# Optimization experiments

Measured on AMD Instinct MI355X. Metric: run time of the kernel, lower is better.

The kernel has to match this reference:

```python
import jax, jax.numpy as jnp
import numpy as np

B, S, U = 64, 64, 16
EMB = 10
D = U - 2 + 2 * EMB      # encoder d_model = 34
DD = 3                   # decoder d_model
FF = 4                   # dim_feedforward
NL = 4                   # num layers (enc and dec)
ENH = 2                  # encoder heads
WV, SV = 10000, 400      # word / syllable vocab sizes


def _ln(x, w, b, eps=1e-5):
    mu = jnp.mean(x, -1, keepdims=True)
    var = jnp.mean((x - mu) ** 2, -1, keepdims=True)
    return (x - mu) / jnp.sqrt(var + eps) * w + b


def _mha(xq, xkv, qkv_w, qkv_b, out_w, out_b, nhead, mask=None):
    d = xq.shape[-1]
    wq, wk, wv = jnp.split(qkv_w, 3, axis=0)
    bq, bk, bv = jnp.split(qkv_b, 3, axis=0)
    q = xq @ wq.T + bq
    k = xkv @ wk.T + bk
    v = xkv @ wv.T + bv
    b_, sq, sk = q.shape[0], q.shape[1], k.shape[1]
    dh = d // nhead
    q = q.reshape(b_, sq, nhead, dh)
    k = k.reshape(b_, sk, nhead, dh)
    v = v.reshape(b_, sk, nhead, dh)
    scores = jnp.einsum('bqhd,bkhd->bhqk', q, k) * (1.0 / np.sqrt(dh))
    if mask is not None:
        scores = scores + mask
    attn = jax.nn.softmax(scores, axis=-1)
    out = jnp.einsum('bhqk,bkhd->bqhd', attn, v).reshape(b_, sq, d)
    return out @ out_w.T + out_b


def _pos_encoding(batch, d_model):
    # Faithful to the original quirk: pe has shape [max_len, 1, d] and is added
    # to a batch-first [B,S,D] tensor as x + pe[:B]  ->  row b of pe is added
    # to ALL sequence positions of batch element b.
    pos = jnp.arange(batch, dtype=jnp.float32)[:, None]
    div = jnp.exp(jnp.arange(0, d_model, 2, dtype=jnp.float32) * (-np.log(10000.0) / d_model))
    ang = pos * div  # [B, D/2]
    pe = jnp.stack([jnp.sin(ang), jnp.cos(ang)], axis=-1).reshape(batch, d_model)
    return pe[:, None, :]  # [B,1,D]


def setup_inputs() -> dict:
    key = jax.random.key(0)
    ks = iter(jax.random.split(key, 64))

    def n(shape, s=0.1):
        return jax.random.normal(next(ks), shape, dtype=jnp.float32) * s

    base = jax.random.uniform(next(ks), (B, S, U), dtype=jnp.float32)
    widx = jax.random.randint(next(ks), (B, S), 0, WV).astype(jnp.float32)
    sidx = jax.random.randint(next(ks), (B, S), 0, SV).astype(jnp.float32)
    src = base.at[:, :, U - 2].set(widx).at[:, :, U - 1].set(sidx)
    return {
        'src': src,
        'word_emb': jax.random.uniform(next(ks), (WV, EMB), jnp.float32, -0.1, 0.1),
        'syll_emb': jax.random.uniform(next(ks), (SV, EMB), jnp.float32, -0.1, 0.1),
        'enc_qkv_w': n((NL, 3 * D, D)), 'enc_qkv_b': jnp.zeros((NL, 3 * D)),
        'enc_out_w': n((NL, D, D)), 'enc_out_b': jnp.zeros((NL, D)),
        'enc_ln1_w': jnp.ones((NL, D)), 'enc_ln1_b': jnp.zeros((NL, D)),
        'enc_lin1_w': n((NL, FF, D)), 'enc_lin1_b': jnp.zeros((NL, FF)),
        'enc_lin2_w': n((NL, D, FF)), 'enc_lin2_b': jnp.zeros((NL, D)),
        'enc_ln2_w': jnp.ones((NL, D)), 'enc_ln2_b': jnp.zeros((NL, D)),
        'norm_w': jnp.ones((D,)), 'norm_b': jnp.zeros((D,)),
        'eo_w': jax.random.uniform(next(ks), (DD, D), jnp.float32, -0.1, 0.1),
        'eo_b': jnp.zeros((DD,)),
        'dec_sa_qkv_w': n((NL, 3 * DD, DD)), 'dec_sa_qkv_b': jnp.zeros((NL, 3 * DD)),
        'dec_sa_out_w': n((NL, DD, DD)), 'dec_sa_out_b': jnp.zeros((NL, DD)),
        'dec_ln1_w': jnp.ones((NL, DD)), 'dec_ln1_b': jnp.zeros((NL, DD)),
        'dec_ca_qkv_w': n((NL, 3 * DD, DD)), 'dec_ca_qkv_b': jnp.zeros((NL, 3 * DD)),
        'dec_ca_out_w': n((NL, DD, DD)), 'dec_ca_out_b': jnp.zeros((NL, DD)),
        'dec_ln2_w': jnp.ones((NL, DD)), 'dec_ln2_b': jnp.zeros((NL, DD)),
        'dec_lin1_w': n((NL, FF, DD)), 'dec_lin1_b': jnp.zeros((NL, FF)),
        'dec_lin2_w': n((NL, DD, FF)), 'dec_lin2_b': jnp.zeros((NL, DD)),
        'dec_ln3_w': jnp.ones((NL, DD)), 'dec_ln3_b': jnp.zeros((NL, DD)),
    }


def reference(src, word_emb, syll_emb,
              enc_qkv_w, enc_qkv_b, enc_out_w, enc_out_b,
              enc_ln1_w, enc_ln1_b, enc_lin1_w, enc_lin1_b,
              enc_lin2_w, enc_lin2_b, enc_ln2_w, enc_ln2_b,
              norm_w, norm_b, eo_w, eo_b,
              dec_sa_qkv_w, dec_sa_qkv_b, dec_sa_out_w, dec_sa_out_b,
              dec_ln1_w, dec_ln1_b,
              dec_ca_qkv_w, dec_ca_qkv_b, dec_ca_out_w, dec_ca_out_b,
              dec_ln2_w, dec_ln2_b,
              dec_lin1_w, dec_lin1_b, dec_lin2_w, dec_lin2_b,
              dec_ln3_w, dec_ln3_b):
    b, s = src.shape[0], src.shape[1]
    # embed_lyrics
    widx = src[:, :, U - 2].astype(jnp.int32)
    sidx = src[:, :, U - 1].astype(jnp.int32)
    x = jnp.concatenate([src[:, :, :U - 2], word_emb[widx], syll_emb[sidx]], axis=2)  # [B,S,D]
    x = x + _pos_encoding(b, D)
    # TransformerEncoder (post-norm, relu, dropout=0) + final LayerNorm
    for l in range(NL):
        sa = _mha(x, x, enc_qkv_w[l], enc_qkv_b[l], enc_out_w[l], enc_out_b[l], ENH)
        x = _ln(x + sa, enc_ln1_w[l], enc_ln1_b[l])
        ff = jax.nn.relu(x @ enc_lin1_w[l].T + enc_lin1_b[l]) @ enc_lin2_w[l].T + enc_lin2_b[l]
        x = _ln(x + ff, enc_ln2_w[l], enc_ln2_b[l])
    x = _ln(x, norm_w, norm_b)
    memory = x @ eo_w.T + eo_b  # [B,S,3]

    causal = jnp.where(jnp.tril(jnp.ones((s, s), bool)), 0.0, -1e9).astype(jnp.float32)

    def decode(tgt):
        y = tgt
        for l in range(NL):
            sa = _mha(y, y, dec_sa_qkv_w[l], dec_sa_qkv_b[l], dec_sa_out_w[l], dec_sa_out_b[l], 1, causal)
            y = _ln(y + sa, dec_ln1_w[l], dec_ln1_b[l])
            ca = _mha(y, memory, dec_ca_qkv_w[l], dec_ca_qkv_b[l], dec_ca_out_w[l], dec_ca_out_b[l], 1)
            y = _ln(y + ca, dec_ln2_w[l], dec_ln2_b[l])
            ff = jax.nn.relu(y @ dec_lin1_w[l].T + dec_lin1_b[l]) @ dec_lin2_w[l].T + dec_lin2_b[l]
            y = _ln(y + ff, dec_ln3_w[l], dec_ln3_b[l])
        return y

    # mask, position i only depends on tgt[:, :i+1], so a fixed-size padded
    # buffer + scan computes identical values.
    def step(tgt, i):
        out_i = jax.lax.dynamic_slice_in_dim(decode(tgt), i, 1, axis=1)  # [B,1,3]
        return jax.lax.dynamic_update_slice(tgt, out_i, (0, i + 1, 0)), None

    tgt0 = jnp.zeros((b, s, DD), jnp.float32)
    tgt, _ = jax.lax.scan(step, tgt0, jnp.arange(s - 1))
    return jnp.concatenate([tgt, src[:, :, U - 2:U - 1], src[:, :, U - 1:U]], axis=2)
```

## Files before the change

kernel.cpp:

```cpp
#include <hip/hip_runtime.h>
#include <math.h>

#define B_ 64
#define S_ 64
#define U_ 16
#define EMB_ 10
#define D_ 34
#define DD_ 3
#define FF_ 4
#define NL_ 4

typedef float v2f __attribute__((ext_vector_type(2)));

__global__ __launch_bounds__(512) void enc_kernel(
    const float* __restrict__ src, const float* __restrict__ wemb,
    const float* __restrict__ semb,
    const float* __restrict__ qkv_w, const float* __restrict__ qkv_b,
    const float* __restrict__ out_w, const float* __restrict__ out_b,
    const float* __restrict__ ln1_w, const float* __restrict__ ln1_b,
    const float* __restrict__ lin1_w, const float* __restrict__ lin1_b,
    const float* __restrict__ lin2_w, const float* __restrict__ lin2_b,
    const float* __restrict__ ln2_w, const float* __restrict__ ln2_b,
    const float* __restrict__ norm_w, const float* __restrict__ norm_b,
    const float* __restrict__ eo_w, const float* __restrict__ eo_b,
    float* __restrict__ mem, float* __restrict__ out)
{
    const int b = blockIdx.x;
    const int tid = threadIdx.x;
    const int wv_ = tid >> 6;
    const int lane = tid & 63;

    __shared__ float xs[S_][D_ + 1];
    __shared__ float tmp[S_][D_ + 1];
    __shared__ float att[S_][D_ + 1];
    __shared__ __align__(16) float qsh[2][S_][21];
    __shared__ __align__(16) float ksh[2][S_][20];
    __shared__ __align__(16) float vsh[2][S_][20];
    __shared__ float ffh[S_][5];
    __shared__ float pacc[4][128][19];

    const float rs17 = 0.24253562503633297f;
    const float negln = -logf(10000.0f) / (float)D_;

    #pragma unroll
    for (int rr = 0; rr < 5; ++rr) {
        int idx = tid + rr * 512;
        if (idx < S_ * D_) {
            int pos = idx / D_, d = idx % D_;
            float v;
            if (d < U_ - 2) {
                v = src[(b * S_ + pos) * U_ + d];
            } else if (d < U_ - 2 + EMB_) {
                int wi = (int)src[(b * S_ + pos) * U_ + (U_ - 2)];
                v = wemb[wi * EMB_ + (d - (U_ - 2))];
            } else {
                int si = (int)src[(b * S_ + pos) * U_ + (U_ - 1)];
                v = semb[si * EMB_ + (d - (U_ - 2 + EMB_))];
            }
            int k = d >> 1;
            float div = __expf((float)(2 * k) * negln);
            float ang = (float)b * div;
            v += (d & 1) ? __cosf(ang) : __sinf(ang);
            xs[pos][d] = v;
        }
    }
    __syncthreads();

    for (int l = 0; l < NL_; ++l) {
        const float* Wq = qkv_w + l * 3 * D_ * D_;
        const float* Bq = qkv_b + l * 3 * D_;

        {
            v2f xr2[17];
            #pragma unroll
            for (int d2 = 0; d2 < 17; ++d2) {
                v2f t; t.x = xs[lane][2 * d2]; t.y = xs[lane][2 * d2 + 1];
                xr2[d2] = t;
            }
            #pragma unroll
            for (int rb = 0; rb < 13; ++rb) {
                int r = wv_ + (rb << 3);
                if (r < 3 * D_) {
                    int ru = __builtin_amdgcn_readfirstlane(r);
                    const v2f* w2 = (const v2f*)(Wq + ru * D_);
                    v2f a2; a2.x = Bq[ru]; a2.y = 0.f;
                    #pragma unroll
                    for (int d2 = 0; d2 < 17; ++d2)
                        a2 = __builtin_elementwise_fma(xr2[d2], w2[d2], a2);
                    float acc = a2.x + a2.y;
                    if (ru < D_)          { int h = (ru >= 17), dd = ru - h * 17; qsh[h][lane][dd] = acc; }
                    else if (ru < 2 * D_) { int rr2 = ru - D_;     int h = (rr2 >= 17), dd = rr2 - h * 17; ksh[h][lane][dd] = acc; }
                    else                  { int rr2 = ru - 2 * D_; int h = (rr2 >= 17), dd = rr2 - h * 17; vsh[h][lane][dd] = acc; }
                }
            }
        }
        __syncthreads();

        {
            int c = tid >> 7, hq = tid & 127;
            int h = hq >> 6, qi = hq & 63;
            float qv[17], acc[17];
            #pragma unroll
            for (int d = 0; d < 17; ++d) { qv[d] = qsh[h][qi][d]; acc[d] = 0.f; }
            float ssum = 0.f;
            int j0 = c * 16;
            #pragma unroll 4
            for (int jj = 0; jj < 16; ++jj) {
                int j = j0 + jj;
                const float4* kr = (const float4*)ksh[h][j];
                const float4* vr = (const float4*)vsh[h][j];
                float4 k0 = kr[0], k1 = kr[1], k2 = kr[2], k3 = kr[3];
                float  k16 = ksh[h][j][16];
                float4 v0 = vr[0], v1 = vr[1], v2 = vr[2], v3 = vr[3];
                float  v16 = vsh[h][j][16];
                float sE = qv[0]*k0.x + qv[2]*k0.z + qv[4]*k1.x + qv[6]*k1.z +
                           qv[8]*k2.x + qv[10]*k2.z + qv[12]*k3.x + qv[14]*k3.z;
                float sO = qv[1]*k0.y + qv[3]*k0.w + qv[5]*k1.y + qv[7]*k1.w +
                           qv[9]*k2.y + qv[11]*k2.w + qv[13]*k3.y + qv[15]*k3.w;
                float sc = sE + sO + qv[16]*k16;
                float e = __expf(sc * rs17);
                ssum += e;
                acc[0] += e*v0.x;  acc[1] += e*v0.y;  acc[2] += e*v0.z;  acc[3] += e*v0.w;
                acc[4] += e*v1.x;  acc[5] += e*v1.y;  acc[6] += e*v1.z;  acc[7] += e*v1.w;
                acc[8] += e*v2.x;  acc[9] += e*v2.y;  acc[10] += e*v2.z; acc[11] += e*v2.w;
                acc[12] += e*v3.x; acc[13] += e*v3.y; acc[14] += e*v3.z; acc[15] += e*v3.w;
                acc[16] += e*v16;
            }
            #pragma unroll
            for (int d = 0; d < 17; ++d) pacc[c][hq][d] = acc[d];
            pacc[c][hq][17] = ssum;
        }
        __syncthreads();

        if (tid < 128) {
            int h = tid >> 6, qi = tid & 63;
            int off = h * 17;
            float ssum = pacc[0][tid][17] + pacc[1][tid][17] +
                         pacc[2][tid][17] + pacc[3][tid][17];
            float inv = 1.f / ssum;
            #pragma unroll
            for (int d = 0; d < 17; ++d)
                att[qi][off + d] = (pacc[0][tid][d] + pacc[1][tid][d] +
                                    pacc[2][tid][d] + pacc[3][tid][d]) * inv;
        }
        __syncthreads();

        {
            v2f ar2[17];
            #pragma unroll
            for (int d2 = 0; d2 < 17; ++d2) {
                v2f t; t.x = att[lane][2 * d2]; t.y = att[lane][2 * d2 + 1];
                ar2[d2] = t;
            }
            const float* Wo = out_w + l * D_ * D_;
            const float* Bo = out_b + l * D_;
            #pragma unroll
            for (int rb = 0; rb < 5; ++rb) {
                int d = wv_ + (rb << 3);
                if (d < D_) {
                    int du = __builtin_amdgcn_readfirstlane(d);
                    const v2f* w2 = (const v2f*)(Wo + du * D_);
                    v2f a2; a2.x = Bo[du]; a2.y = 0.f;
                    #pragma unroll
                    for (int d2 = 0; d2 < 17; ++d2)
                        a2 = __builtin_elementwise_fma(ar2[d2], w2[d2], a2);
                    tmp[lane][du] = xs[lane][du] + a2.x + a2.y;
                }
            }
        }
        __syncthreads();

        {
            int row = tid >> 3, sub = tid & 7;
            float s = 0.f, sq = 0.f;
            #pragma unroll
            for (int d = sub; d < D_; d += 8) { float t = tmp[row][d]; s += t; sq = fmaf(t, t, sq); }
            #pragma unroll
            for (int m = 1; m < 8; m <<= 1) { s += __shfl_xor(s, m, 8); sq += __shfl_xor(sq, m, 8); }
            float mu = s * (1.0f / D_);
            float var = fmaf(sq, 1.0f / D_, -mu * mu);
            float rstd = rsqrtf(var + 1e-5f);
            #pragma unroll
            for (int d = sub; d < D_; d += 8)
                xs[row][d] = (tmp[row][d] - mu) * rstd * ln1_w[l * D_ + d] + ln1_b[l * D_ + d];
        }
        __syncthreads();

        if (wv_ < 4) {
            int fu = __builtin_amdgcn_readfirstlane(wv_);
            const v2f* w2 = (const v2f*)(lin1_w + l * FF_ * D_ + fu * D_);
            v2f a2; a2.x = lin1_b[l * FF_ + fu]; a2.y = 0.f;
            #pragma unroll
            for (int d2 = 0; d2 < 17; ++d2) {
                v2f t; t.x = xs[lane][2 * d2]; t.y = xs[lane][2 * d2 + 1];
                a2 = __builtin_elementwise_fma(t, w2[d2], a2);
            }
            ffh[lane][fu] = fmaxf(a2.x + a2.y, 0.f);
        }
        __syncthreads();

        {
            float h0 = ffh[lane][0], h1 = ffh[lane][1],
                  h2 = ffh[lane][2], h3 = ffh[lane][3];
            const float* W2 = lin2_w + l * D_ * FF_;
            const float* B2 = lin2_b + l * D_;
            #pragma unroll
            for (int rb = 0; rb < 5; ++rb) {
                int d = wv_ + (rb << 3);
                if (d < D_) {
                    int du = __builtin_amdgcn_readfirstlane(d);
                    const float* wrow = W2 + du * FF_;
                    float acc = fmaf(h0, wrow[0], fmaf(h1, wrow[1],
                                fmaf(h2, wrow[2], fmaf(h3, wrow[3], B2[du]))));
                    tmp[lane][du] = xs[lane][du] + acc;
                }
            }
        }
        __syncthreads();

        {
            int row = tid >> 3, sub = tid & 7;
            float s = 0.f, sq = 0.f;
            #pragma unroll
            for (int d = sub; d < D_; d += 8) { float t = tmp[row][d]; s += t; sq = fmaf(t, t, sq); }
            #pragma unroll
            for (int m = 1; m < 8; m <<= 1) { s += __shfl_xor(s, m, 8); sq += __shfl_xor(sq, m, 8); }
            float mu = s * (1.0f / D_);
            float var = fmaf(sq, 1.0f / D_, -mu * mu);
            float rstd = rsqrtf(var + 1e-5f);
            #pragma unroll
            for (int d = sub; d < D_; d += 8)
                xs[row][d] = (tmp[row][d] - mu) * rstd * ln2_w[l * D_ + d] + ln2_b[l * D_ + d];
        }
        __syncthreads();
    }

    {
        int row = tid >> 3, sub = tid & 7;
        float s = 0.f, sq = 0.f;
        #pragma unroll
        for (int d = sub; d < D_; d += 8) { float t = xs[row][d]; s += t; sq = fmaf(t, t, sq); }
        #pragma unroll
        for (int m = 1; m < 8; m <<= 1) { s += __shfl_xor(s, m, 8); sq += __shfl_xor(sq, m, 8); }
        float mu = s * (1.0f / D_);
        float var = fmaf(sq, 1.0f / D_, -mu * mu);
        float rstd = rsqrtf(var + 1e-5f);
        #pragma unroll
        for (int d = sub; d < D_; d += 8)
            tmp[row][d] = (xs[row][d] - mu) * rstd * norm_w[d] + norm_b[d];
    }
    __syncthreads();

    if (wv_ < 3) {
        int ru = __builtin_amdgcn_readfirstlane(wv_);
        const v2f* w2 = (const v2f*)(eo_w + ru * D_);
        v2f a2; a2.x = eo_b[ru]; a2.y = 0.f;
        #pragma unroll
        for (int d2 = 0; d2 < 17; ++d2) {
            v2f t; t.x = tmp[lane][2 * d2]; t.y = tmp[lane][2 * d2 + 1];
            a2 = __builtin_elementwise_fma(t, w2[d2], a2);
        }
        mem[(b * S_ + lane) * DD_ + ru] = a2.x + a2.y;
    }

    if (tid < S_) {
        out[(b * S_ + tid) * 5 + 3] = src[(b * S_ + tid) * U_ + (U_ - 2)];
        out[(b * S_ + tid) * 5 + 4] = src[(b * S_ + tid) * U_ + (U_ - 1)];
    }
}

#define PIN(x) asm volatile("" : "+v"(x))

template <int N> struct IC { static constexpr int value = N; };

template <int CTRL>
__device__ __forceinline__ void dpp4(float& a, float& b, float& c, float& d) {
    int ta = __builtin_amdgcn_update_dpp(0, __float_as_int(a), CTRL, 0xf, 0xf, true);
    int tb = __builtin_amdgcn_update_dpp(0, __float_as_int(b), CTRL, 0xf, 0xf, true);
    int tc = __builtin_amdgcn_update_dpp(0, __float_as_int(c), CTRL, 0xf, 0xf, true);
    int td = __builtin_amdgcn_update_dpp(0, __float_as_int(d), CTRL, 0xf, 0xf, true);
    a += __int_as_float(ta);
    b += __int_as_float(tb);
    c += __int_as_float(tc);
    d += __int_as_float(td);
}

__device__ __forceinline__ void red16_4(float& a, float& b, float& c, float& d) {
    dpp4<0x111>(a, b, c, d);
    dpp4<0x112>(a, b, c, d);
    dpp4<0x114>(a, b, c, d);
    dpp4<0x118>(a, b, c, d);
}

template <int L>
__device__ __forceinline__ float rlane(float v) {
    return __int_as_float(__builtin_amdgcn_readlane(__float_as_int(v), L));
}

__device__ __forceinline__ void ln3e(float z0, float z1, float z2,
                                     float w0, float w1, float w2,
                                     float b0, float b1, float b2,
                                     float& o0, float& o1, float& o2) {
    float s1 = (z0 + z1) + z2;
    float s2 = fmaf(z0, z0, fmaf(z1, z1, z2 * z2));
    float mu = s1 * (1.0f / 3.0f);
    float vpe = fmaf(s2, (1.0f / 3.0f), fmaf(-mu, mu, 1e-5f));
    float rstd = __builtin_amdgcn_rsqf(vpe);
    o0 = fmaf(z0 - mu, rstd * w0, b0);
    o1 = fmaf(z1 - mu, rstd * w1, b1);
    o2 = fmaf(z2 - mu, rstd * w2, b2);
}

__global__ __launch_bounds__(64, 1) void dec_kernel(
    const float* __restrict__ mem,
    const float* __restrict__ sa_qkv_w, const float* __restrict__ sa_qkv_b,
    const float* __restrict__ sa_out_w, const float* __restrict__ sa_out_b,
    const float* __restrict__ gln1_w, const float* __restrict__ gln1_b,
    const float* __restrict__ ca_qkv_w, const float* __restrict__ ca_qkv_b,
    const float* __restrict__ ca_out_w, const float* __restrict__ ca_out_b,
    const float* __restrict__ gln2_w, const float* __restrict__ gln2_b,
    const float* __restrict__ l1_w, const float* __restrict__ l1_b,
    const float* __restrict__ l2_w, const float* __restrict__ l2_b,
    const float* __restrict__ gln3_w, const float* __restrict__ gln3_b,
    float* __restrict__ out)
{
    const int b = blockIdx.x;
    const int lane = threadIdx.x;
    const float LOG2E = 1.4426950408889634f;
    const float rs3 = 0.5773502691896258f;
    const float QS = rs3 * LOG2E;

    __shared__ __align__(16) float fst[NL_][40];
    for (int t = lane; t < NL_ * 40; t += 64) {
        int l = t / 40, s = t % 40;
        float v = 0.f;
        if      (s < 12) v = l1_w[l * 12 + s] * gln2_w[l * 3 + (s % 3)];
        else if (s < 16) {
            int j = s - 12;
            v = l1_w[l * 12 + j * 3 + 0] * gln2_b[l * 3 + 0] +
                l1_w[l * 12 + j * 3 + 1] * gln2_b[l * 3 + 1] +
                l1_w[l * 12 + j * 3 + 2] * gln2_b[l * 3 + 2] + l1_b[l * 4 + j];
        }
        else if (s < 28) v = l2_w[l * 12 + (s - 16)];
        else if (s < 31) v = l2_b[l * 3 + (s - 28)];
        else if (s < 34) v = gln3_w[l * 3 + (s - 31)];
        else if (s < 37) v = gln3_b[l * 3 + (s - 34)];
        fst[l][s] = v;
    }
    __syncthreads();

    float Wsq[NL_][9][3], Bsq[NL_][9];
    float Wso[NL_][3][3], Bso[NL_][3];
    float N1w[NL_][3], N1b[NL_][3];
    float N2w[NL_][3], N2b[NL_][3];
    float Bco[NL_][3];
    float wcu[NL_][3];
    float swcu[NL_];
    float cbb[NL_];
    float cvp[NL_][3];

    #pragma unroll
    for (int l = 0; l < NL_; ++l) {
        #pragma unroll
        for (int r = 0; r < 9; ++r) {
            float sc = (r < 3) ? QS : 1.0f;
            Bsq[l][r] = sa_qkv_b[l * 9 + r] * sc;
            #pragma unroll
            for (int c = 0; c < 3; ++c) Wsq[l][r][c] = sa_qkv_w[l * 27 + r * 3 + c] * sc;
        }
        #pragma unroll
        for (int r = 0; r < 3; ++r) {
            Bso[l][r] = sa_out_b[l * 3 + r];
            Bco[l][r] = ca_out_b[l * 3 + r];
            N1w[l][r] = gln1_w[l * 3 + r];  N1b[l][r] = gln1_b[l * 3 + r];
            N2w[l][r] = gln2_w[l * 3 + r];  N2b[l][r] = gln2_b[l * 3 + r];
            #pragma unroll
            for (int c = 0; c < 3; ++c) Wso[l][r][c] = sa_out_w[l * 9 + r * 3 + c];
        }
    }

    float m0 = mem[(b * S_ + lane) * DD_ + 0];
    float m1 = mem[(b * S_ + lane) * DD_ + 1];
    float m2 = mem[(b * S_ + lane) * DD_ + 2];

    #pragma unroll
    for (int l = 0; l < NL_; ++l) {
        float ck[3], cv[3], cuv[3];
        #pragma unroll
        for (int r = 0; r < 3; ++r) {
            ck[r] = ca_qkv_w[l * 27 + (3 + r) * 3 + 0] * m0 +
                    ca_qkv_w[l * 27 + (3 + r) * 3 + 1] * m1 +
                    ca_qkv_w[l * 27 + (3 + r) * 3 + 2] * m2 + ca_qkv_b[l * 9 + 3 + r];
            cv[r] = ca_qkv_w[l * 27 + (6 + r) * 3 + 0] * m0 +
                    ca_qkv_w[l * 27 + (6 + r) * 3 + 1] * m1 +
                    ca_qkv_w[l * 27 + (6 + r) * 3 + 2] * m2 + ca_qkv_b[l * 9 + 6 + r];
        }
        #pragma unroll
        for (int s = 0; s < 3; ++s)
            cuv[s] = QS * (ca_qkv_w[l * 27 + 0 + s] * ck[0] +
                           ca_qkv_w[l * 27 + 3 + s] * ck[1] +
                           ca_qkv_w[l * 27 + 6 + s] * ck[2]);
        float cbv = QS * (ca_qkv_b[l * 9 + 0] * ck[0] +
                          ca_qkv_b[l * 9 + 1] * ck[1] +
                          ca_qkv_b[l * 9 + 2] * ck[2]);
        #pragma unroll
        for (int r = 0; r < 3; ++r)
            cvp[l][r] = ca_out_w[l * 9 + r * 3 + 0] * cv[0] +
                        ca_out_w[l * 9 + r * 3 + 1] * cv[1] +
                        ca_out_w[l * 9 + r * 3 + 2] * cv[2];
        #pragma unroll
        for (int r = 0; r < 3; ++r) wcu[l][r] = cuv[r] * N1w[l][r];
        swcu[l] = wcu[l][0] + wcu[l][1] + wcu[l][2];
        cbb[l]  = cbv + cuv[0] * N1b[l][0] + cuv[1] * N1b[l][1] + cuv[2] * N1b[l][2];
    }

    #pragma unroll
    for (int l = 0; l < NL_; ++l) {
        #pragma unroll
        for (int r = 0; r < 9; ++r) {
            PIN(Bsq[l][r]);
            #pragma unroll
            for (int c = 0; c < 3; ++c) PIN(Wsq[l][r][c]);
        }
        PIN(swcu[l]); PIN(cbb[l]);
        #pragma unroll
        for (int r = 0; r < 3; ++r) {
            PIN(Bso[l][r]); PIN(Bco[l][r]);
            PIN(N1w[l][r]); PIN(N1b[l][r]); PIN(N2w[l][r]); PIN(N2b[l][r]);
            PIN(wcu[l][r]); PIN(cvp[l][r]);
            #pragma unroll
            for (int c = 0; c < 3; ++c) PIN(Wso[l][r][c]);
        }
    }

    float sk[NL_][3] = {{0.f}}, sv[NL_][3] = {{0.f}};

    if (lane < 3) out[(b * S_ + 0) * 5 + lane] = 0.f;

    float y0 = 0.f, y1 = 0.f, y2 = 0.f;

    auto run_range = [&](int ibeg, int iend, auto nstc) {
        constexpr int NST = decltype(nstc)::value;
        constexpr int RL = (NST == 4) ? 15 : (NST == 5) ? 31 : 63;
        for (int i = ibeg; i < iend; ++i) {
            float msa = (lane <= i) ? 0.f : -1.0e30f;
            bool isme = (lane == i);
            #pragma unroll
            for (int l = 0; l < NL_; ++l) {
                float wv[40];
                {
                    const float4* fp = (const float4*)fst[l];
                    #pragma unroll
                    for (int k = 0; k < 10; ++k) {
                        float4 t4 = fp[k];
                        wv[4 * k + 0] = t4.x; wv[4 * k + 1] = t4.y;
                        wv[4 * k + 2] = t4.z; wv[4 * k + 3] = t4.w;
                    }
                }

                float q[3], kn[3], vn[3], vp[3];
                #pragma unroll
                for (int r = 0; r < 3; ++r) {
                    kn[r] = fmaf(Wsq[l][3 + r][0], y0, fmaf(Wsq[l][3 + r][1], y1, fmaf(Wsq[l][3 + r][2], y2, Bsq[l][3 + r])));
                    q[r]  = fmaf(Wsq[l][r][0], y0, fmaf(Wsq[l][r][1], y1, fmaf(Wsq[l][r][2], y2, Bsq[l][r])));
                    vn[r] = fmaf(Wsq[l][6 + r][0], y0, fmaf(Wsq[l][6 + r][1], y1, fmaf(Wsq[l][6 + r][2], y2, Bsq[l][6 + r])));
                }
                #pragma unroll
                for (int r = 0; r < 3; ++r)
                    vp[r] = fmaf(Wso[l][r][0], vn[0], fmaf(Wso[l][r][1], vn[1], Wso[l][r][2] * vn[2]));
                if (isme) {
                    #pragma unroll
                    for (int r = 0; r < 3; ++r) { sk[l][r] = kn[r]; sv[l][r] = vp[r]; }
                }
                float sc = fmaf(q[0], sk[l][0], fmaf(q[1], sk[l][1], fmaf(q[2], sk[l][2], msa)));
                float e = __builtin_amdgcn_exp2f(sc);
                float se = e;
                float sa0 = e * sv[l][0];
                float sa1 = e * sv[l][1];
                float sa2 = e * sv[l][2];
                red16_4(se, sa0, sa1, sa2);
                if constexpr (NST >= 5) dpp4<0x142>(se, sa0, sa1, sa2);
                if constexpr (NST >= 6) dpp4<0x143>(se, sa0, sa1, sa2);
                float es = rlane<RL>(se);
                float S0 = rlane<RL>(sa0), S1 = rlane<RL>(sa1), S2 = rlane<RL>(sa2);
                float yb0 = y0 + Bso[l][0], yb1 = y1 + Bso[l][1], yb2 = y2 + Bso[l][2];
                float z0 = fmaf(yb0, es, S0), z1 = fmaf(yb1, es, S1), z2v = fmaf(yb2, es, S2);
                float ee = es * es;

                float s1m = (z0 + z1) + z2v;
                float mu = s1m * (1.0f / 3.0f);
                float zw = fmaf(z0, wcu[l][0], fmaf(z1, wcu[l][1], z2v * wcu[l][2]));
                float inner = fmaf(-mu, swcu[l], zw);
                float s2m = fmaf(z0, z0, fmaf(z1, z1, z2v * z2v));
                float vpe = fmaf(s2m, (1.0f / 3.0f), fmaf(-mu, mu, 1e-5f * ee));
                float rstd1 = __builtin_amdgcn_rsqf(vpe);
                float sc2 = fmaf(rstd1, inner, cbb[l]);
                float e2 = __builtin_amdgcn_exp2f(sc2);
                float ce = e2;
                float ca0 = e2 * cvp[l][0];
                float ca1 = e2 * cvp[l][1];
                float ca2 = e2 * cvp[l][2];
                red16_4(ce, ca0, ca1, ca2);
                dpp4<0x142>(ce, ca0, ca1, ca2);
                dpp4<0x143>(ce, ca0, ca1, ca2);
                float y1_0 = fmaf(z0 - mu, rstd1 * N1w[l][0], N1b[l][0]);
                float y1_1 = fmaf(z1 - mu, rstd1 * N1w[l][1], N1b[l][1]);
                float y1_2 = fmaf(z2v - mu, rstd1 * N1w[l][2], N1b[l][2]);
                float yc0 = y1_0 + Bco[l][0], yc1 = y1_1 + Bco[l][1], yc2 = y1_2 + Bco[l][2];
                float cs = rlane<63>(ce);
                float C0 = rlane<63>(ca0), C1 = rlane<63>(ca1), C2 = rlane<63>(ca2);
                float g0 = fmaf(yc0, cs, C0), g1 = fmaf(yc1, cs, C1), g2 = fmaf(yc2, cs, C2);
                float cee = cs * cs;

                float t1m = (g0 + g1) + g2;
                float mu2 = t1m * (1.0f / 3.0f);
                float c20 = g0 - mu2, c21 = g1 - mu2, c22 = g2 - mu2;
                float t2m = fmaf(g0, g0, fmaf(g1, g1, g2 * g2));
                float vpe2 = fmaf(t2m, (1.0f / 3.0f), fmaf(-mu2, mu2, 1e-5f * cee));
                float rstd2 = __builtin_amdgcn_rsqf(vpe2);
                #pragma unroll
                for (int k = 0; k < 37; ++k) PIN(wv[k]);
                float d0 = fmaf(wv[0], c20, fmaf(wv[1],  c21, wv[2]  * c22));
                float d1 = fmaf(wv[3], c20, fmaf(wv[4],  c21, wv[5]  * c22));
                float d2 = fmaf(wv[6], c20, fmaf(wv[7],  c21, wv[8]  * c22));
                float d3 = fmaf(wv[9], c20, fmaf(wv[10], c21, wv[11] * c22));
                float h0 = fmaxf(fmaf(rstd2, d0, wv[12]), 0.f);
                float h1 = fmaxf(fmaf(rstd2, d1, wv[13]), 0.f);
                float h2 = fmaxf(fmaf(rstd2, d2, wv[14]), 0.f);
                float h3 = fmaxf(fmaf(rstd2, d3, wv[15]), 0.f);
                float y2_0 = fmaf(c20, rstd2 * N2w[l][0], N2b[l][0]);
                float y2_1 = fmaf(c21, rstd2 * N2w[l][1], N2b[l][1]);
                float y2_2 = fmaf(c22, rstd2 * N2w[l][2], N2b[l][2]);
                float yf0 = y2_0 + wv[28], yf1 = y2_1 + wv[29], yf2 = y2_2 + wv[30];
                float f0 = fmaf(wv[16], h0, fmaf(wv[17], h1, fmaf(wv[18], h2, fmaf(wv[19], h3, yf0))));
                float f1 = fmaf(wv[20], h0, fmaf(wv[21], h1, fmaf(wv[22], h2, fmaf(wv[23], h3, yf1))));
                float f2 = fmaf(wv[24], h0, fmaf(wv[25], h1, fmaf(wv[26], h2, fmaf(wv[27], h3, yf2))));
                ln3e(f0, f1, f2,
                     wv[31], wv[32], wv[33], wv[34], wv[35], wv[36],
                     y0, y1, y2);
            }
            if (lane == 0) {
                out[(b * S_ + i + 1) * 5 + 0] = y0;
                out[(b * S_ + i + 1) * 5 + 1] = y1;
                out[(b * S_ + i + 1) * 5 + 2] = y2;
            }
        }
    };

    run_range(0, 15, IC<4>{});
    run_range(15, 31, IC<5>{});
    run_range(31, S_ - 1, IC<6>{});
}

extern "C" void kernel_launch(void* const* d_in, const int* in_sizes, int n_in,
                              void* d_out, int out_size, void* d_ws, size_t ws_size,
                              hipStream_t stream) {
    const float* src  = (const float*)d_in[0];
    const float* wemb = (const float*)d_in[1];
    const float* semb = (const float*)d_in[2];

    float* mem = (float*)d_ws;
    float* out = (float*)d_out;

    enc_kernel<<<B_, 512, 0, stream>>>(
        src, wemb, semb,
        (const float*)d_in[3],  (const float*)d_in[4],
        (const float*)d_in[5],  (const float*)d_in[6],
        (const float*)d_in[7],  (const float*)d_in[8],
        (const float*)d_in[9],  (const float*)d_in[10],
        (const float*)d_in[11], (const float*)d_in[12],
        (const float*)d_in[13], (const float*)d_in[14],
        (const float*)d_in[15], (const float*)d_in[16],
        (const float*)d_in[17], (const float*)d_in[18],
        mem, out);

    dec_kernel<<<B_, 64, 0, stream>>>(
        mem,
        (const float*)d_in[19], (const float*)d_in[20],
        (const float*)d_in[21], (const float*)d_in[22],
        (const float*)d_in[23], (const float*)d_in[24],
        (const float*)d_in[25], (const float*)d_in[26],
        (const float*)d_in[27], (const float*)d_in[28],
        (const float*)d_in[29], (const float*)d_in[30],
        (const float*)d_in[31], (const float*)d_in[32],
        (const float*)d_in[33], (const float*)d_in[34],
        (const float*)d_in[35], (const float*)d_in[36],
        out);
}
```

Measured before the change: 322.2 us.

## Pack four batch elements per decoder wave with 16-lane DPP row reductions

The decoder kernel now maps four batch elements onto one 64-lane wave, 16 lanes each, with every lane holding four sequence positions of the cross- and self-attention keys and values. Softmax sums become a per-lane partial over four positions followed by a 16-lane all-reduce built from quad_perm and row mirror DPP ops. This replaces the longer cross-row DPP chain plus readlane broadcasts on the serial per-token critical path, and removes the three range-specialised loop copies. In exchange each lane computes four exponentials per attention, register pressure rises, and the grid shrinks to 16 blocks.

Measured after the change: 423.4 us. +31.4%, slower.

```diff
diff --git a/kernel.cpp b/kernel.cpp
--- a/kernel.cpp
+++ b/kernel.cpp
@@ -271,8 +271,6 @@
 
 #define PIN(x) asm volatile("" : "+v"(x))
 
-template <int N> struct IC { static constexpr int value = N; };
-
 template <int CTRL>
 __device__ __forceinline__ void dpp4(float& a, float& b, float& c, float& d) {
     int ta = __builtin_amdgcn_update_dpp(0, __float_as_int(a), CTRL, 0xf, 0xf, true);
@@ -285,16 +283,11 @@
     d += __int_as_float(td);
 }
 
-__device__ __forceinline__ void red16_4(float& a, float& b, float& c, float& d) {
-    dpp4<0x111>(a, b, c, d);
-    dpp4<0x112>(a, b, c, d);
-    dpp4<0x114>(a, b, c, d);
-    dpp4<0x118>(a, b, c, d);
-}
-
-template <int L>
-__device__ __forceinline__ float rlane(float v) {
-    return __int_as_float(__builtin_amdgcn_readlane(__float_as_int(v), L));
+__device__ __forceinline__ void hsum16_4(float& a, float& b, float& c, float& d) {
+    dpp4<0xB1>(a, b, c, d);
+    dpp4<0x4E>(a, b, c, d);
+    dpp4<0x141>(a, b, c, d);
+    dpp4<0x140>(a, b, c, d);
 }
 
 __device__ __forceinline__ void ln3e(float z0, float z1, float z2,
@@ -324,8 +317,10 @@
     const float* __restrict__ gln3_w, const float* __restrict__ gln3_b,
     float* __restrict__ out)
 {
-    const int b = blockIdx.x;
+    const int b0 = blockIdx.x * 4;
     const int lane = threadIdx.x;
+    const int grp = lane >> 4, j16 = lane & 15;
+    const int bb = b0 + grp;
     const float LOG2E = 1.4426950408889634f;
     const float rs3 = 0.5773502691896258f;
     const float QS = rs3 * LOG2E;
@@ -354,10 +349,10 @@
     float N1w[NL_][3], N1b[NL_][3];
     float N2w[NL_][3], N2b[NL_][3];
     float Bco[NL_][3];
-    float wcu[NL_][3];
-    float swcu[NL_];
-    float cbb[NL_];
-    float cvp[NL_][3];
+    float wcu[4][NL_][3];
+    float swcu[4][NL_];
+    float cbb[4][NL_];
+    float cvp[4][NL_][3];
 
     #pragma unroll
     for (int l = 0; l < NL_; ++l) {
@@ -379,177 +374,190 @@
         }
     }
 
-    float m0 = mem[(b * S_ + lane) * DD_ + 0];
-    float m1 = mem[(b * S_ + lane) * DD_ + 1];
-    float m2 = mem[(b * S_ + lane) * DD_ + 2];
+    #pragma unroll
+    for (int s4 = 0; s4 < 4; ++s4) {
+        float m0 = mem[(bb * S_ + s4 * 16 + j16) * DD_ + 0];
+        float m1 = mem[(bb * S_ + s4 * 16 + j16) * DD_ + 1];
+        float m2 = mem[(bb * S_ + s4 * 16 + j16) * DD_ + 2];
+        #pragma unroll
+        for (int l = 0; l < NL_; ++l) {
+            float ck[3], cv[3], cuv[3];
+            #pragma unroll
+            for (int r = 0; r < 3; ++r) {
+                ck[r] = ca_qkv_w[l * 27 + (3 + r) * 3 + 0] * m0 +
+                        ca_qkv_w[l * 27 + (3 + r) * 3 + 1] * m1 +
+                        ca_qkv_w[l * 27 + (3 + r) * 3 + 2] * m2 + ca_qkv_b[l * 9 + 3 + r];
+                cv[r] = ca_qkv_w[l * 27 + (6 + r) * 3 + 0] * m0 +
+                        ca_qkv_w[l * 27 + (6 + r) * 3 + 1] * m1 +
+                        ca_qkv_w[l * 27 + (6 + r) * 3 + 2] * m2 + ca_qkv_b[l * 9 + 6 + r];
+            }
+            #pragma unroll
+            for (int s = 0; s < 3; ++s)
+                cuv[s] = QS * (ca_qkv_w[l * 27 + 0 + s] * ck[0] +
+                               ca_qkv_w[l * 27 + 3 + s] * ck[1] +
+                               ca_qkv_w[l * 27 + 6 + s] * ck[2]);
+            float cbv = QS * (ca_qkv_b[l * 9 + 0] * ck[0] +
+                              ca_qkv_b[l * 9 + 1] * ck[1] +
+                              ca_qkv_b[l * 9 + 2] * ck[2]);
+            #pragma unroll
+            for (int r = 0; r < 3; ++r)
+                cvp[s4][l][r] = ca_out_w[l * 9 + r * 3 + 0] * cv[0] +
+                                ca_out_w[l * 9 + r * 3 + 1] * cv[1] +
+                                ca_out_w[l * 9 + r * 3 + 2] * cv[2];
+            #pragma unroll
+            for (int r = 0; r < 3; ++r) wcu[s4][l][r] = cuv[r] * N1w[l][r];
+            swcu[s4][l] = wcu[s4][l][0] + wcu[s4][l][1] + wcu[s4][l][2];
+            cbb[s4][l]  = cbv + cuv[0] * N1b[l][0] + cuv[1] * N1b[l][1] + cuv[2] * N1b[l][2];
+        }
+    }
 
     #pragma unroll
     for (int l = 0; l < NL_; ++l) {
-        float ck[3], cv[3], cuv[3];
-        #pragma unroll
-        for (int r = 0; r < 3; ++r) {
-            ck[r] = ca_qkv_w[l * 27 + (3 + r) * 3 + 0] * m0 +
-                    ca_qkv_w[l * 27 + (3 + r) * 3 + 1] * m1 +
-                    ca_qkv_w[l * 27 + (3 + r) * 3 + 2] * m2 + ca_qkv_b[l * 9 + 3 + r];
-            cv[r] = ca_qkv_w[l * 27 + (6 + r) * 3 + 0] * m0 +
-                    ca_qkv_w[l * 27 + (6 + r) * 3 + 1] * m1 +
-                    ca_qkv_w[l * 27 + (6 + r) * 3 + 2] * m2 + ca_qkv_b[l * 9 + 6 + r];
-        }
-        #pragma unroll
-        for (int s = 0; s < 3; ++s)
-            cuv[s] = QS * (ca_qkv_w[l * 27 + 0 + s] * ck[0] +
-                           ca_qkv_w[l * 27 + 3 + s] * ck[1] +
-                           ca_qkv_w[l * 27 + 6 + s] * ck[2]);
-        float cbv = QS * (ca_qkv_b[l * 9 + 0] * ck[0] +
-                          ca_qkv_b[l * 9 + 1] * ck[1] +
-                          ca_qkv_b[l * 9 + 2] * ck[2]);
-        #pragma unroll
-        for (int r = 0; r < 3; ++r)
-            cvp[l][r] = ca_out_w[l * 9 + r * 3 + 0] * cv[0] +
-                        ca_out_w[l * 9 + r * 3 + 1] * cv[1] +
-                        ca_out_w[l * 9 + r * 3 + 2] * cv[2];
-        #pragma unroll
-        for (int r = 0; r < 3; ++r) wcu[l][r] = cuv[r] * N1w[l][r];
-        swcu[l] = wcu[l][0] + wcu[l][1] + wcu[l][2];
-        cbb[l]  = cbv + cuv[0] * N1b[l][0] + cuv[1] * N1b[l][1] + cuv[2] * N1b[l][2];
-    }
-
-    #pragma unroll
-    for (int l = 0; l < NL_; ++l) {
         #pragma unroll
         for (int r = 0; r < 9; ++r) {
             PIN(Bsq[l][r]);
             #pragma unroll
             for (int c = 0; c < 3; ++c) PIN(Wsq[l][r][c]);
         }
-        PIN(swcu[l]); PIN(cbb[l]);
         #pragma unroll
         for (int r = 0; r < 3; ++r) {
             PIN(Bso[l][r]); PIN(Bco[l][r]);
             PIN(N1w[l][r]); PIN(N1b[l][r]); PIN(N2w[l][r]); PIN(N2b[l][r]);
-            PIN(wcu[l][r]); PIN(cvp[l][r]);
             #pragma unroll
             for (int c = 0; c < 3; ++c) PIN(Wso[l][r][c]);
         }
-    }
-
-    float sk[NL_][3] = {{0.f}}, sv[NL_][3] = {{0.f}};
-
-    if (lane < 3) out[(b * S_ + 0) * 5 + lane] = 0.f;
+        #pragma unroll
+        for (int s4 = 0; s4 < 4; ++s4) {
+            PIN(swcu[s4][l]); PIN(cbb[s4][l]);
+            #pragma unroll
+            for (int r = 0; r < 3; ++r) { PIN(wcu[s4][l][r]); PIN(cvp[s4][l][r]); }
+        }
+    }
+
+    float sk[4][NL_][3] = {{{0.f}}}, sv[4][NL_][3] = {{{0.f}}};
+
+    if (j16 < 3) out[(bb * S_ + 0) * 5 + j16] = 0.f;
 
     float y0 = 0.f, y1 = 0.f, y2 = 0.f;
 
-    auto run_range = [&](int ibeg, int iend, auto nstc) {
-        constexpr int NST = decltype(nstc)::value;
-        constexpr int RL = (NST == 4) ? 15 : (NST == 5) ? 31 : 63;
-        for (int i = ibeg; i < iend; ++i) {
-            float msa = (lane <= i) ? 0.f : -1.0e30f;
-            bool isme = (lane == i);
-            #pragma unroll
-            for (int l = 0; l < NL_; ++l) {
-                float wv[40];
-                {
-                    const float4* fp = (const float4*)fst[l];
+    for (int i = 0; i < S_ - 1; ++i) {
+        float msa[4];
+        #pragma unroll
+        for (int s = 0; s < 4; ++s)
+            msa[s] = (s * 16 + j16 <= i) ? 0.f : -1.0e30f;
+        bool lm = (j16 == (i & 15));
+
+        #pragma unroll
+        for (int l = 0; l < NL_; ++l) {
+            float wv[40];
+            {
+                const float4* fp = (const float4*)fst[l];
+                #pragma unroll
+                for (int k = 0; k < 10; ++k) {
+                    float4 t4 = fp[k];
+                    wv[4 * k + 0] = t4.x; wv[4 * k + 1] = t4.y;
+                    wv[4 * k + 2] = t4.z; wv[4 * k + 3] = t4.w;
+                }
+            }
+
+            float q[3], kn[3], vn[3], vp[3];
+            #pragma unroll
+            for (int r = 0; r < 3; ++r) {
+                kn[r] = fmaf(Wsq[l][3 + r][0], y0, fmaf(Wsq[l][3 + r][1], y1, fmaf(Wsq[l][3 + r][2], y2, Bsq[l][3 + r])));
+                q[r]  = fmaf(Wsq[l][r][0], y0, fmaf(Wsq[l][r][1], y1, fmaf(Wsq[l][r][2], y2, Bsq[l][r])));
+                vn[r] = fmaf(Wsq[l][6 + r][0], y0, fmaf(Wsq[l][6 + r][1], y1, fmaf(Wsq[l][6 + r][2], y2, Bsq[l][6 + r])));
+            }
+            #pragma unroll
+            for (int r = 0; r < 3; ++r)
+                vp[r] = fmaf(Wso[l][r][0], vn[0], fmaf(Wso[l][r][1], vn[1], Wso[l][r][2] * vn[2]));
+            if (lm) {
+                if (i < 16) {
                     #pragma unroll
-                    for (int k = 0; k < 10; ++k) {
-                        float4 t4 = fp[k];
-                        wv[4 * k + 0] = t4.x; wv[4 * k + 1] = t4.y;
-                        wv[4 * k + 2] = t4.z; wv[4 * k + 3] = t4.w;
-                    }
+                    for (int r = 0; r < 3; ++r) { sk[0][l][r] = kn[r]; sv[0][l][r] = vp[r]; }
+                } else if (i < 32) {
+                    #pragma unroll
+                    for (int r = 0; r < 3; ++r) { sk[1][l][r] = kn[r]; sv[1][l][r] = vp[r]; }
+                } else if (i < 48) {
+                    #pragma unroll
+                    for (int r = 0; r < 3; ++r) { sk[2][l][r] = kn[r]; sv[2][l][r] = vp[r]; }
+                } else {
+                    #pragma unroll
+                    for (int r = 0; r < 3; ++r) { sk[3][l][r] = kn[r]; sv[3][l][r] = vp[r]; }
                 }
-
-                float q[3], kn[3], vn[3], vp[3];
-                #pragma unroll
-                for (int r = 0; r < 3; ++r) {
-                    kn[r] = fmaf(Wsq[l][3 + r][0], y0, fmaf(Wsq[l][3 + r][1], y1, fmaf(Wsq[l][3 + r][2], y2, Bsq[l][3 + r])));
-                    q[r]  = fmaf(Wsq[l][r][0], y0, fmaf(Wsq[l][r][1], y1, fmaf(Wsq[l][r][2], y2, Bsq[l][r])));
-                    vn[r] = fmaf(Wsq[l][6 + r][0], y0, fmaf(Wsq[l][6 + r][1], y1, fmaf(Wsq[l][6 + r][2], y2, Bsq[l][6 + r])));
-                }
-                #pragma unroll
-                for (int r = 0; r < 3; ++r)
-                    vp[r] = fmaf(Wso[l][r][0], vn[0], fmaf(Wso[l][r][1], vn[1], Wso[l][r][2] * vn[2]));
-                if (isme) {
-                    #pragma unroll
-                    for (int r = 0; r < 3; ++r) { sk[l][r] = kn[r]; sv[l][r] = vp[r]; }
-                }
-                float sc = fmaf(q[0], sk[l][0], fmaf(q[1], sk[l][1], fmaf(q[2], sk[l][2], msa)));
-                float e = __builtin_amdgcn_exp2f(sc);
-                float se = e;
-                float sa0 = e * sv[l][0];
-                float sa1 = e * sv[l][1];
-                float sa2 = e * sv[l][2];
-                red16_4(se, sa0, sa1, sa2);
-                if constexpr (NST >= 5) dpp4<0x142>(se, sa0, sa1, sa2);
-                if constexpr (NST >= 6) dpp4<0x143>(se, sa0, sa1, sa2);
-                float es = rlane<RL>(se);
-                float S0 = rlane<RL>(sa0), S1 = rlane<RL>(sa1), S2 = rlane<RL>(sa2);
-                float yb0 = y0 + Bso[l][0], yb1 = y1 + Bso[l][1], yb2 = y2 + Bso[l][2];
-                float z0 = fmaf(yb0, es, S0), z1 = fmaf(yb1, es, S1), z2v = fmaf(yb2, es, S2);
-                float ee = es * es;
-
-                float s1m = (z0 + z1) + z2v;
-                float mu = s1m * (1.0f / 3.0f);
-                float zw = fmaf(z0, wcu[l][0], fmaf(z1, wcu[l][1], z2v * wcu[l][2]));
-                float inner = fmaf(-mu, swcu[l], zw);
-                float s2m = fmaf(z0, z0, fmaf(z1, z1, z2v * z2v));
-                float vpe = fmaf(s2m, (1.0f / 3.0f), fmaf(-mu, mu, 1e-5f * ee));
-                float rstd1 = __builtin_amdgcn_rsqf(vpe);
-                float sc2 = fmaf(rstd1, inner, cbb[l]);
-                float e2 = __builtin_amdgcn_exp2f(sc2);
-                float ce = e2;
-                float ca0 = e2 * cvp[l][0];
-                float ca1 = e2 * cvp[l][1];
-                float ca2 = e2 * cvp[l][2];
-                red16_4(ce, ca0, ca1, ca2);
-                dpp4<0x142>(ce, ca0, ca1, ca2);
-                dpp4<0x143>(ce, ca0, ca1, ca2);
-                float y1_0 = fmaf(z0 - mu, rstd1 * N1w[l][0], N1b[l][0]);
-                float y1_1 = fmaf(z1 - mu, rstd1 * N1w[l][1], N1b[l][1]);
-                float y1_2 = fmaf(z2v - mu, rstd1 * N1w[l][2], N1b[l][2]);
-                float yc0 = y1_0 + Bco[l][0], yc1 = y1_1 + Bco[l][1], yc2 = y1_2 + Bco[l][2];
-                float cs = rlane<63>(ce);
-                float C0 = rlane<63>(ca0), C1 = rlane<63>(ca1), C2 = rlane<63>(ca2);
-                float g0 = fmaf(yc0, cs, C0), g1 = fmaf(yc1, cs, C1), g2 = fmaf(yc2, cs, C2);
-                float cee = cs * cs;
-
-                float t1m = (g0 + g1) + g2;
-                float mu2 = t1m * (1.0f / 3.0f);
-                float c20 = g0 - mu2, c21 = g1 - mu2, c22 = g2 - mu2;
-                float t2m = fmaf(g0, g0, fmaf(g1, g1, g2 * g2));
-                float vpe2 = fmaf(t2m, (1.0f / 3.0f), fmaf(-mu2, mu2, 1e-5f * cee));
-                float rstd2 = __builtin_amdgcn_rsqf(vpe2);
-                #pragma unroll
-                for (int k = 0; k < 37; ++k) PIN(wv[k]);
-                float d0 = fmaf(wv[0], c20, fmaf(wv[1],  c21, wv[2]  * c22));
-                float d1 = fmaf(wv[3], c20, fmaf(wv[4],  c21, wv[5]  * c22));
-                float d2 = fmaf(wv[6], c20, fmaf(wv[7],  c21, wv[8]  * c22));
-                float d3 = fmaf(wv[9], c20, fmaf(wv[10], c21, wv[11] * c22));
-                float h0 = fmaxf(fmaf(rstd2, d0, wv[12]), 0.f);
-                float h1 = fmaxf(fmaf(rstd2, d1, wv[13]), 0.f);
-                float h2 = fmaxf(fmaf(rstd2, d2, wv[14]), 0.f);
-                float h3 = fmaxf(fmaf(rstd2, d3, wv[15]), 0.f);
-                float y2_0 = fmaf(c20, rstd2 * N2w[l][0], N2b[l][0]);
-                float y2_1 = fmaf(c21, rstd2 * N2w[l][1], N2b[l][1]);
-                float y2_2 = fmaf(c22, rstd2 * N2w[l][2], N2b[l][2]);
-                float yf0 = y2_0 + wv[28], yf1 = y2_1 + wv[29], yf2 = y2_2 + wv[30];
-                float f0 = fmaf(wv[16], h0, fmaf(wv[17], h1, fmaf(wv[18], h2, fmaf(wv[19], h3, yf0))));
-                float f1 = fmaf(wv[20], h0, fmaf(wv[21], h1, fmaf(wv[22], h2, fmaf(wv[23], h3, yf1))));
-                float f2 = fmaf(wv[24], h0, fmaf(wv[25], h1, fmaf(wv[26], h2, fmaf(wv[27], h3, yf2))));
-                ln3e(f0, f1, f2,
-                     wv[31], wv[32], wv[33], wv[34], wv[35], wv[36],
-                     y0, y1, y2);
-            }
-            if (lane == 0) {
-                out[(b * S_ + i + 1) * 5 + 0] = y0;
-                out[(b * S_ + i + 1) * 5 + 1] = y1;
-                out[(b * S_ + i + 1) * 5 + 2] = y2;
-            }
-        }
-    };
-
-    run_range(0, 15, IC<4>{});
-    run_range(15, 31, IC<5>{});
-    run_range(31, S_ - 1, IC<6>{});
+            }
+            float e_[4];
+            #pragma unroll
+            for (int s = 0; s < 4; ++s) {
+                float sc = fmaf(q[0], sk[s][l][0], fmaf(q[1], sk[s][l][1], fmaf(q[2], sk[s][l][2], msa[s])));
+                e_[s] = __builtin_amdgcn_exp2f(sc);
+            }
+            float se = (e_[0] + e_[1]) + (e_[2] + e_[3]);
+            float S0 = fmaf(e_[3], sv[3][l][0], fmaf(e_[2], sv[2][l][0], fmaf(e_[1], sv[1][l][0], e_[0] * sv[0][l][0])));
+            float S1 = fmaf(e_[3], sv[3][l][1], fmaf(e_[2], sv[2][l][1], fmaf(e_[1], sv[1][l][1], e_[0] * sv[0][l][1])));
+            float S2 = fmaf(e_[3], sv[3][l][2], fmaf(e_[2], sv[2][l][2], fmaf(e_[1], sv[1][l][2], e_[0] * sv[0][l][2])));
+            hsum16_4(se, S0, S1, S2);
+            float yb0 = y0 + Bso[l][0], yb1 = y1 + Bso[l][1], yb2 = y2 + Bso[l][2];
+            float z0 = fmaf(yb0, se, S0), z1 = fmaf(yb1, se, S1), z2v = fmaf(yb2, se, S2);
+            float ee = se * se;
+
+            float s1m = (z0 + z1) + z2v;
+            float mu = s1m * (1.0f / 3.0f);
+            float s2m = fmaf(z0, z0, fmaf(z1, z1, z2v * z2v));
+            float vpe = fmaf(s2m, (1.0f / 3.0f), fmaf(-mu, mu, 1e-5f * ee));
+            float rstd1 = __builtin_amdgcn_rsqf(vpe);
+            float e2_[4];
+            #pragma unroll
+            for (int s = 0; s < 4; ++s) {
+                float zw = fmaf(z0, wcu[s][l][0], fmaf(z1, wcu[s][l][1], z2v * wcu[s][l][2]));
+                float inner = fmaf(-mu, swcu[s][l], zw);
+                float sc2 = fmaf(rstd1, inner, cbb[s][l]);
+                e2_[s] = __builtin_amdgcn_exp2f(sc2);
+            }
+            float ce = (e2_[0] + e2_[1]) + (e2_[2] + e2_[3]);
+            float C0 = fmaf(e2_[3], cvp[3][l][0], fmaf(e2_[2], cvp[2][l][0], fmaf(e2_[1], cvp[1][l][0], e2_[0] * cvp[0][l][0])));
+            float C1 = fmaf(e2_[3], cvp[3][l][1], fmaf(e2_[2], cvp[2][l][1], fmaf(e2_[1], cvp[1][l][1], e2_[0] * cvp[0][l][1])));
+            float C2 = fmaf(e2_[3], cvp[3][l][2], fmaf(e2_[2], cvp[2][l][2], fmaf(e2_[1], cvp[1][l][2], e2_[0] * cvp[0][l][2])));
+            hsum16_4(ce, C0, C1, C2);
+            float y1_0 = fmaf(z0 - mu, rstd1 * N1w[l][0], N1b[l][0]);
+            float y1_1 = fmaf(z1 - mu, rstd1 * N1w[l][1], N1b[l][1]);
+            float y1_2 = fmaf(z2v - mu, rstd1 * N1w[l][2], N1b[l][2]);
+            float yc0 = y1_0 + Bco[l][0], yc1 = y1_1 + Bco[l][1], yc2 = y1_2 + Bco[l][2];
+            float g0 = fmaf(yc0, ce, C0), g1 = fmaf(yc1, ce, C1), g2 = fmaf(yc2, ce, C2);
+            float cee = ce * ce;
+
+            float t1m = (g0 + g1) + g2;
+            float mu2 = t1m * (1.0f / 3.0f);
+            float c20 = g0 - mu2, c21 = g1 - mu2, c22 = g2 - mu2;
+            float t2m = fmaf(g0, g0, fmaf(g1, g1, g2 * g2));
+            float vpe2 = fmaf(t2m, (1.0f / 3.0f), fmaf(-mu2, mu2, 1e-5f * cee));
+            float rstd2 = __builtin_amdgcn_rsqf(vpe2);
+            #pragma unroll
+            for (int k = 0; k < 37; ++k) PIN(wv[k]);
+            float d0 = fmaf(wv[0], c20, fmaf(wv[1],  c21, wv[2]  * c22));
+            float d1 = fmaf(wv[3], c20, fmaf(wv[4],  c21, wv[5]  * c22));
+            float d2 = fmaf(wv[6], c20, fmaf(wv[7],  c21, wv[8]  * c22));
+            float d3 = fmaf(wv[9], c20, fmaf(wv[10], c21, wv[11] * c22));
+            float h0 = fmaxf(fmaf(rstd2, d0, wv[12]), 0.f);
+            float h1 = fmaxf(fmaf(rstd2, d1, wv[13]), 0.f);
+            float h2 = fmaxf(fmaf(rstd2, d2, wv[14]), 0.f);
+            float h3 = fmaxf(fmaf(rstd2, d3, wv[15]), 0.f);
+            float y2_0 = fmaf(c20, rstd2 * N2w[l][0], N2b[l][0]);
+            float y2_1 = fmaf(c21, rstd2 * N2w[l][1], N2b[l][1]);
+            float y2_2 = fmaf(c22, rstd2 * N2w[l][2], N2b[l][2]);
+            float yf0 = y2_0 + wv[28], yf1 = y2_1 + wv[29], yf2 = y2_2 + wv[30];
+            float f0 = fmaf(wv[16], h0, fmaf(wv[17], h1, fmaf(wv[18], h2, fmaf(wv[19], h3, yf0))));
+            float f1 = fmaf(wv[20], h0, fmaf(wv[21], h1, fmaf(wv[22], h2, fmaf(wv[23], h3, yf1))));
+            float f2 = fmaf(wv[24], h0, fmaf(wv[25], h1, fmaf(wv[26], h2, fmaf(wv[27], h3, yf2))));
+            ln3e(f0, f1, f2,
+                 wv[31], wv[32], wv[33], wv[34], wv[35], wv[36],
+                 y0, y1, y2);
+        }
+        if (j16 == 0) {
+            out[(bb * S_ + i + 1) * 5 + 0] = y0;
+            out[(bb * S_ + i + 1) * 5 + 1] = y1;
+            out[(bb * S_ + i + 1) * 5 + 2] = y2;
+        }
+    }
 }
 
 extern "C" void kernel_launch(void* const* d_in, const int* in_sizes, int n_in,
@@ -574,7 +582,7 @@
         (const float*)d_in[17], (const float*)d_in[18],
         mem, out);
 
-    dec_kernel<<<B_, 64, 0, stream>>>(
+    dec_kernel<<<B_ / 4, 64, 0, stream>>>(
         mem,
         (const float*)d_in[19], (const float*)d_in[20],
         (const float*)d_in[21], (const float*)d_in[22],
```
